# Kernel tuning notes

Measured on AMD Instinct MI355X. Metric: run time of the kernel, lower is better.

The kernel has to match this reference:

```python
import jax, jax.numpy as jnp
import numpy as np

B = 512      # batch
F = 512      # n_features
G = 32       # grid_size
N = G * G    # num_nodes = 1024
D = 64       # embed_dim
H = 64       # hidden_dim
C = 100      # n_classes
A = 8        # num_atoms in symbiotic basis
EPS = 1e-8
DEG_EPS = 1e-6


def _grid_mask():
    """4-neighborhood mask for a GxG grid, [N, N] float32."""
    m = np.zeros((N, N), dtype=np.float32)
    for i in range(N):
        r, c = divmod(i, G)
        if r > 0:
            m[i, i - G] = 1.0
        if r < G - 1:
            m[i, i + G] = 1.0
        if c > 0:
            m[i, i - 1] = 1.0
        if c < G - 1:
            m[i, i + 1] = 1.0
    return jnp.asarray(m)


def setup_inputs() -> dict:
    key = jax.random.key(0)
    ks = jax.random.split(key, 16)
    s = 0.05  # small init scale (stands in for kaiming init)
    return {
        "x": jax.random.normal(ks[0], (B, F), jnp.float32),
        "W_embed": jax.random.normal(ks[1], (F, N * D), jnp.float32) * s,
        "b_embed": jnp.zeros((N * D,), jnp.float32),
        "adj_weights": jax.random.normal(ks[2], (N, N), jnp.float32) * 0.1,
        "adj_mask": _grid_mask(),
        "W1": jax.random.normal(ks[3], (D, H), jnp.float32) * s,
        "b1": jnp.zeros((H,), jnp.float32),
        "W2": jax.random.normal(ks[4], (H, D), jnp.float32) * s,
        "b2": jnp.zeros((D,), jnp.float32),
        "basis": jax.random.normal(ks[5], (A, D), jnp.float32) * 0.5,
        "Wq": jax.random.normal(ks[6], (D, D), jnp.float32) * s,
        "Wk": jax.random.normal(ks[7], (D, D), jnp.float32) * s,
        "Wr1": jax.random.normal(ks[8], (N * D, 2 * H), jnp.float32) * s,
        "br1": jnp.zeros((2 * H,), jnp.float32),
        "Wr2": jax.random.normal(ks[9], (2 * H, C), jnp.float32) * s,
        "br2": jnp.zeros((C,), jnp.float32),
    }


def _gelu(v):
    return jax.nn.gelu(v, approximate=False)  # torch nn.GELU default (erf)


def reference(x, W_embed, b_embed, adj_weights, adj_mask, W1, b1, W2, b2,
              basis, Wq, Wk, Wr1, br1, Wr2, br2):
    plasticity = 1.0
    bsz = x.shape[0]
    # input embed -> [B, N, D]
    x_embed = (x @ W_embed + b_embed).reshape(bsz, N, D)
    # dynamic topology: sigmoid-gated, mask-multiplied, degree-normalized adjacency
    adj = jax.nn.sigmoid(adj_weights * plasticity) * adj_mask          # [N, N]
    deg = jnp.clip(adj.sum(axis=1, keepdims=True), DEG_EPS, None)
    adj = adj / deg
    # graph diffusion (shared adjacency across batch)
    x_agg = jnp.einsum('ij,bjd->bid', adj, x_embed)                    # [B, N, D]
    # node processor MLP
    x_proc = _gelu(x_agg @ W1 + b1) @ W2 + b2                          # [B, N, D]
    # symbiotic basis refinement on flattened rows [B*N, D]
    flat = x_proc.reshape(-1, D)
    Q = flat @ Wq                                                      # [B*N, D]
    K = basis @ Wk                                                     # [A, D]
    attn = (Q @ K.T) / (jnp.sqrt(jnp.float32(D)) + EPS)                # [B*N, A]
    weights = jax.nn.softmax(attn, axis=-1)
    x_clean = jnp.clip(weights @ basis, -5.0, 5.0)                     # [B*N, D]
    w_safe = weights + EPS
    entropy = -(w_safe * jnp.log(w_safe)).sum(-1).mean()
    gram = basis @ basis.T
    ortho = jnp.clip(jnp.sum((gram - jnp.eye(A, dtype=gram.dtype)) ** 2), 0.0, 10.0)
    # readout (dropout is identity in eval)
    x_flat = x_clean.reshape(bsz, N * D)
    logits = _gelu(x_flat @ Wr1 + br1) @ Wr2 + br2                     # [B, C]
    return (logits, entropy, ortho)
```

## Files before the change

kernel.cpp:

```cpp
#include <hip/hip_runtime.h>
#include <hip/hip_bf16.h>
#include <math.h>

#define Bb 512
#define Ff 512
#define Gg 32
#define Nn 1024
#define Dd 64
#define Hh 64
#define Cc 100
#define Aa 8
#define NDd 65536

typedef float  f32x4  __attribute__((ext_vector_type(4)));
typedef __bf16 bf16x8 __attribute__((ext_vector_type(8)));

static __device__ __forceinline__ unsigned short f2bf(float f) {
    __bf16 h = (__bf16)f;
    return __builtin_bit_cast(unsigned short, h);
}
static __device__ __forceinline__ float gelu_f(float v) {
    return 0.5f * v * (1.0f + erff(v * 0.7071067811865476f));
}
static __device__ __forceinline__ float gelu_fast(float v) {
    float z = 1.5957691216057308f * v * (1.0f + 0.044715f * v * v);
    return v / (1.0f + __expf(-z));
}
static __device__ __forceinline__ float sigm(float v) {
    return 1.0f / (1.0f + expf(-v));
}

__global__ void k_adj(const float* __restrict__ aw, const float* __restrict__ be,
                      float* __restrict__ adjw, float* __restrict__ be_agg) {
    int i = blockIdx.x * 256 + threadIdx.x;
    if (i >= Nn) return;
    int r = i >> 5, c = i & 31;
    float s0 = 0.f, s1 = 0.f, s2 = 0.f, s3 = 0.f;
    if (r > 0)       s0 = sigm(aw[(size_t)i * Nn + i - Gg]);
    if (r < Gg - 1)  s1 = sigm(aw[(size_t)i * Nn + i + Gg]);
    if (c > 0)       s2 = sigm(aw[(size_t)i * Nn + i - 1]);
    if (c < Gg - 1)  s3 = sigm(aw[(size_t)i * Nn + i + 1]);
    float deg = fmaxf(s0 + s1 + s2 + s3, 1e-6f);
    float inv = 1.0f / deg;
    float w0 = s0 * inv, w1 = s1 * inv, w2 = s2 * inv, w3 = s3 * inv;
    adjw[i * 4 + 0] = w0;
    adjw[i * 4 + 1] = w1;
    adjw[i * 4 + 2] = w2;
    adjw[i * 4 + 3] = w3;
    int nu = max(i - 32, 0), nd = min(i + 32, 1023);
    int nl = max(i - 1, 0),  nr = min(i + 1, 1023);
    #pragma unroll 4
    for (int d4 = 0; d4 < 16; ++d4) {
        f32x4 vu = *(const f32x4*)(be + nu * 64 + d4 * 4);
        f32x4 vd = *(const f32x4*)(be + nd * 64 + d4 * 4);
        f32x4 vl = *(const f32x4*)(be + nl * 64 + d4 * 4);
        f32x4 vr = *(const f32x4*)(be + nr * 64 + d4 * 4);
        f32x4 o = w0 * vu + w1 * vd + w2 * vl + w3 * vr;
        *(f32x4*)(be_agg + i * 64 + d4 * 4) = o;
    }
}

__global__ void __launch_bounds__(512) k_prep(
        const float* __restrict__ W1, const float* __restrict__ b2,
        const float* __restrict__ W2, const float* __restrict__ Wq,
        const float* __restrict__ Wk, const float* __restrict__ basis,
        unsigned short* __restrict__ Kbf, float* __restrict__ bq,
        unsigned short* __restrict__ W1f, unsigned short* __restrict__ Wcf,
        float* __restrict__ ortho_out) {
    __shared__ float sb[Aa * Dd];
    __shared__ float sWc[Hh * Dd];
    __shared__ float sKb[Aa * Dd];
    int t = threadIdx.x;
    sb[t] = basis[t];
    __syncthreads();
    {
        int a = t >> 6, d = t & 63;
        float acc = 0.f;
        #pragma unroll 8
        for (int e = 0; e < Dd; ++e) acc += sb[a * 64 + e] * Wk[e * 64 + d];
        sKb[t] = acc;
    }
    for (int it = 0; it < 8; ++it) {
        int o = it * 512 + t;
        int i = o >> 6, j = o & 63;
        float acc = 0.f;
        #pragma unroll 8
        for (int e = 0; e < 64; ++e) acc += W2[i * 64 + e] * Wq[e * 64 + j];
        sWc[o] = acc;
    }
    if (t < 64) {
        float acc = 0.f;
        #pragma unroll 8
        for (int e = 0; e < 64; ++e) acc += b2[e] * Wq[e * 64 + t];
        bq[t] = acc;
    }
    __syncthreads();
    {
        int l = t & 63, ni = (t >> 6) & 3, kk = t >> 8;
        int col = ni * 16 + (l & 15);
        int kbase = kk * 32 + (l >> 4) * 8;
        #pragma unroll
        for (int j = 0; j < 8; ++j) {
            int k = kbase + j;
            W1f[t * 8 + j] = f2bf(W1[k * 64 + col]);
            Wcf[t * 8 + j] = f2bf(sWc[k * 64 + col]);
        }
    }
    if (t < 128) {
        int lane = t & 63;
        int a = lane & 15;
        int dbase = ((t >> 6) * 32) + (lane >> 4) * 8;
        unsigned short kp[8];
        #pragma unroll
        for (int j = 0; j < 8; ++j)
            kp[j] = (a < 8) ? f2bf(sKb[a * 64 + dbase + j] * 0.125f) : (unsigned short)0;
        *(int4*)(Kbf + (size_t)t * 8) = *(int4*)kp;
    }
    if (t < 64) {
        int i = t >> 3, j = t & 7;
        float gsum = 0.f;
        #pragma unroll 8
        for (int d = 0; d < 64; ++d) gsum += sb[i * 64 + d] * sb[j * 64 + d];
        float diff = gsum - (i == j ? 1.0f : 0.0f);
        float v = diff * diff;
        #pragma unroll
        for (int off = 32; off; off >>= 1) v += __shfl_down(v, off);
        if (t == 0) *ortho_out = fminf(fmaxf(v, 0.0f), 10.0f);
    }
}

__global__ void __launch_bounds__(128) k_prepBW(
        const float* __restrict__ basis, const float* __restrict__ Wr1,
        unsigned short* __restrict__ BWf) {
    __shared__ float sb[Aa * Dd];
    int t = threadIdx.x;
    sb[t] = basis[t];         sb[t + 128] = basis[t + 128];
    sb[t + 256] = basis[t + 256]; sb[t + 384] = basis[t + 384];
    __syncthreads();
    int n = blockIdx.x;
    float acc[8] = {0, 0, 0, 0, 0, 0, 0, 0};
    const float* wr = Wr1 + (size_t)n * 64 * 128 + t;
    for (int d = 0; d < 64; ++d) {
        float v = wr[(size_t)d * 128];
        #pragma unroll
        for (int a = 0; a < 8; ++a) acc[a] += sb[a * 64 + d] * v;
    }
    unsigned short p[8];
    #pragma unroll
    for (int a = 0; a < 8; ++a) p[a] = f2bf(acc[a]);
    int ni = t >> 4, l15 = t & 15;
    *(int4*)(BWf + ((size_t)(((n >> 2) * 8 + ni) * 64) + (n & 3) * 16 + l15) * 8)
        = *(int4*)p;
}

__global__ void __launch_bounds__(256) k_xf(const float* __restrict__ x,
                                            unsigned short* __restrict__ xf) {
    int gid = blockIdx.x * 256 + threadIdx.x;
    int lane = gid & 63, slot = gid >> 6;
    int rt = slot >> 4, kk = slot & 15;
    int row = rt * 16 + (lane & 15), k0 = kk * 32 + (lane >> 4) * 8;
    const float* p = x + (size_t)row * Ff + k0;
    f32x4 v0 = *(const f32x4*)p;
    f32x4 v1 = *(const f32x4*)(p + 4);
    unsigned short o[8];
    o[0] = f2bf(v0.x); o[1] = f2bf(v0.y); o[2] = f2bf(v0.z); o[3] = f2bf(v0.w);
    o[4] = f2bf(v1.x); o[5] = f2bf(v1.y); o[6] = f2bf(v1.z); o[7] = f2bf(v1.w);
    *(int4*)(xf + (size_t)gid * 8) = *(int4*)o;
}

__global__ void __launch_bounds__(256) k_aggW(
        const float* __restrict__ We, const float* __restrict__ adjw,
        unsigned short* __restrict__ AfG) {
    int bid = blockIdx.x;
    int vid = (bid & 7) * 512 + (bid >> 3);
    int fo = vid >> 6;
    int win = vid & 63;
    int t = threadIdx.x;
    int c4 = win * 1024 + t * 4;
    int n = c4 >> 6;
    int d = c4 & 63;
    f32x4 w4 = *(const f32x4*)(adjw + n * 4);
    int nu = max(n - 32, 0), ndn = min(n + 32, 1023);
    int nl = max(n - 1, 0),  nr = min(n + 1, 1023);
    f32x4 vu[8], vd[8], vl[8], vr[8];
    #pragma unroll
    for (int j = 0; j < 8; ++j) {
        const float* row = We + (size_t)(fo * 8 + j) * NDd;
        vu[j] = *(const f32x4*)(row + nu * 64 + d);
        vd[j] = *(const f32x4*)(row + ndn * 64 + d);
        vl[j] = *(const f32x4*)(row + nl * 64 + d);
        vr[j] = *(const f32x4*)(row + nr * 64 + d);
    }
    unsigned short pk[4][8];
    #pragma unroll
    for (int j = 0; j < 8; ++j) {
        f32x4 o4 = w4.x * vu[j] + w4.y * vd[j] + w4.z * vl[j] + w4.w * vr[j];
        pk[0][j] = f2bf(o4.x); pk[1][j] = f2bf(o4.y);
        pk[2][j] = f2bf(o4.z); pk[3][j] = f2bf(o4.w);
    }
    int kk = fo >> 2, l4g = fo & 3;
    int mi = (c4 >> 4) & 3, l15b = c4 & 15;
    size_t base = ((((size_t)n * 16 + kk) * 4 + mi) * 64 + l4g * 16 + l15b) * 8;
    #pragma unroll
    for (int i = 0; i < 4; ++i)
        *(int4*)(AfG + base + i * 8) = *(int4*)pk[i];
}

__global__ void __launch_bounds__(512, 4) k_mega(
        const unsigned short* __restrict__ AfG, const unsigned short* __restrict__ xf,
        const float* __restrict__ be_agg,
        const unsigned short* __restrict__ W1f, const unsigned short* __restrict__ Wcf,
        const float* __restrict__ b1, const float* __restrict__ bq,
        const unsigned short* __restrict__ Kbf,
        unsigned short* __restrict__ w_outT, float* __restrict__ ent_part) {
    __shared__ __align__(16) unsigned short sm[32768];
    int t = threadIdx.x;
    int n = blockIdx.x;
    {
        const int4* src = (const int4*)AfG + (size_t)n * 4096;
        int4* dst = (int4*)sm;
        #pragma unroll
        for (int i = 0; i < 8; ++i) dst[t + i * 512] = src[t + i * 512];
    }
    __syncthreads();
    int lane = t & 63, w = t >> 6;
    int l15 = lane & 15, g = lane >> 4;
    int bs = w * 64;

    f32x4 acc[4][4] = {};
    #pragma unroll 4
    for (int kk = 0; kk < 16; ++kk) {
        bf16x8 a[4], b[4];
        #pragma unroll
        for (int mi = 0; mi < 4; ++mi)
            a[mi] = *(const bf16x8*)(sm + ((kk * 4 + mi) * 64 + lane) * 8);
        #pragma unroll
        for (int ni = 0; ni < 4; ++ni)
            b[ni] = *(const bf16x8*)(xf + ((size_t)(((w * 4 + ni) * 16 + kk) * 64 + lane)) * 8);
        #pragma unroll
        for (int mi = 0; mi < 4; ++mi)
            #pragma unroll
            for (int ni = 0; ni < 4; ++ni)
                acc[mi][ni] = __builtin_amdgcn_mfma_f32_16x16x32_bf16(
                    a[mi], b[ni], acc[mi][ni], 0, 0, 0);
    }
    __syncthreads();
    unsigned short* tile = sm + w * 4096;

    #pragma unroll
    for (int mi = 0; mi < 4; ++mi) {
        f32x4 bv = *(const f32x4*)(be_agg + n * 64 + mi * 16 + g * 4);
        int kk2 = mi >> 1;
        int gt  = ((mi & 1) << 1) + (g >> 1);
        int jb  = (g & 1) << 2;
        #pragma unroll
        for (int ni = 0; ni < 4; ++ni) {
            float v0 = acc[mi][ni][0] + bv[0];
            float v1 = acc[mi][ni][1] + bv[1];
            float v2 = acc[mi][ni][2] + bv[2];
            float v3 = acc[mi][ni][3] + bv[3];
            unsigned d0 = (unsigned)f2bf(v0) | ((unsigned)f2bf(v1) << 16);
            unsigned d1 = (unsigned)f2bf(v2) | ((unsigned)f2bf(v3) << 16);
            int base = ((kk2 * 4 + ni) * 64 + gt * 16 + l15) * 8 + jb;
            *(unsigned*)(tile + base)     = d0;
            *(unsigned*)(tile + base + 2) = d1;
        }
    }

    f32x4 acc1[4][4] = {};
    #pragma unroll
    for (int kk = 0; kk < 2; ++kk) {
        bf16x8 bf4[4];
        #pragma unroll
        for (int ni = 0; ni < 4; ++ni)
            bf4[ni] = *(const bf16x8*)(tile + ((kk * 4 + ni) * 64 + lane) * 8);
        #pragma unroll
        for (int mi = 0; mi < 4; ++mi) {
            bf16x8 aW = *(const bf16x8*)(W1f + ((kk * 4 + mi) * 64 + lane) * 8);
            #pragma unroll
            for (int ni = 0; ni < 4; ++ni)
                acc1[mi][ni] = __builtin_amdgcn_mfma_f32_16x16x32_bf16(
                    aW, bf4[ni], acc1[mi][ni], 0, 0, 0);
        }
    }
    #pragma unroll
    for (int mi = 0; mi < 4; ++mi) {
        f32x4 bv = *(const f32x4*)(b1 + mi * 16 + g * 4);
        int kk2 = mi >> 1;
        int gt  = ((mi & 1) << 1) + (g >> 1);
        int jb  = (g & 1) << 2;
        #pragma unroll
        for (int ni = 0; ni < 4; ++ni) {
            float h0 = gelu_fast(acc1[mi][ni][0] + bv[0]);
            float h1 = gelu_fast(acc1[mi][ni][1] + bv[1]);
            float h2 = gelu_fast(acc1[mi][ni][2] + bv[2]);
            float h3 = gelu_fast(acc1[mi][ni][3] + bv[3]);
            unsigned d0 = (unsigned)f2bf(h0) | ((unsigned)f2bf(h1) << 16);
            unsigned d1 = (unsigned)f2bf(h2) | ((unsigned)f2bf(h3) << 16);
            int base = ((kk2 * 4 + ni) * 64 + gt * 16 + l15) * 8 + jb;
            *(unsigned*)(tile + base)     = d0;
            *(unsigned*)(tile + base + 2) = d1;
        }
    }

    f32x4 acc2[4][4] = {};
    #pragma unroll
    for (int kk = 0; kk < 2; ++kk) {
        bf16x8 bf4[4];
        #pragma unroll
        for (int ni = 0; ni < 4; ++ni)
            bf4[ni] = *(const bf16x8*)(tile + ((kk * 4 + ni) * 64 + lane) * 8);
        #pragma unroll
        for (int mi = 0; mi < 4; ++mi) {
            bf16x8 aW = *(const bf16x8*)(Wcf + ((kk * 4 + mi) * 64 + lane) * 8);
            #pragma unroll
            for (int ni = 0; ni < 4; ++ni)
                acc2[mi][ni] = __builtin_amdgcn_mfma_f32_16x16x32_bf16(
                    aW, bf4[ni], acc2[mi][ni], 0, 0, 0);
        }
    }
    #pragma unroll
    for (int mi = 0; mi < 4; ++mi) {
        f32x4 bv = *(const f32x4*)(bq + mi * 16 + g * 4);
        int kk2 = mi >> 1;
        int gt  = ((mi & 1) << 1) + (g >> 1);
        int jb  = (g & 1) << 2;
        #pragma unroll
        for (int ni = 0; ni < 4; ++ni) {
            float q0 = acc2[mi][ni][0] + bv[0];
            float q1 = acc2[mi][ni][1] + bv[1];
            float q2 = acc2[mi][ni][2] + bv[2];
            float q3 = acc2[mi][ni][3] + bv[3];
            unsigned d0 = (unsigned)f2bf(q0) | ((unsigned)f2bf(q1) << 16);
            unsigned d1 = (unsigned)f2bf(q2) | ((unsigned)f2bf(q3) << 16);
            int base = ((kk2 * 4 + ni) * 64 + gt * 16 + l15) * 8 + jb;
            *(unsigned*)(tile + base)     = d0;
            *(unsigned*)(tile + base + 2) = d1;
        }
    }

    f32x4 accA[4] = {};
    #pragma unroll
    for (int kk = 0; kk < 2; ++kk) {
        bf16x8 kf = *(const bf16x8*)(Kbf + (kk * 64 + lane) * 8);
        #pragma unroll
        for (int ni = 0; ni < 4; ++ni) {
            bf16x8 qf = *(const bf16x8*)(tile + ((kk * 4 + ni) * 64 + lane) * 8);
            accA[ni] = __builtin_amdgcn_mfma_f32_16x16x32_bf16(kf, qf, accA[ni], 0, 0, 0);
        }
    }

    float ent_local = 0.f;
    bool odd = (g & 1);
    #pragma unroll
    for (int ni = 0; ni < 4; ++ni) {
        float xr[4];
        #pragma unroll
        for (int r = 0; r < 4; ++r) xr[r] = __shfl_xor(accA[ni][r], 16);
        float f[8];
        #pragma unroll
        for (int r = 0; r < 4; ++r) {
            f[r]     = odd ? xr[r] : accA[ni][r];
            f[r + 4] = odd ? accA[ni][r] : xr[r];
        }
        float mx = f[0];
        #pragma unroll
        for (int i = 1; i < 8; ++i) mx = fmaxf(mx, f[i]);
        float e[8], S = 0.f, T = 0.f;
        #pragma unroll
        for (int i = 0; i < 8; ++i) {
            e[i] = __expf(f[i] - mx);
            S += e[i];
            T += e[i] * (f[i] - mx);
        }
        float inv = 1.0f / S;
        if (g == 0) {
            ent_local += __logf(S) - T * inv;
            unsigned short pk[8];
            #pragma unroll
            for (int i = 0; i < 8; ++i) pk[i] = f2bf(e[i] * inv);
            *(int4*)(w_outT + ((size_t)n * 512 + bs + ni * 16 + l15) * 8) = *(int4*)pk;
        }
    }
    #pragma unroll
    for (int off = 32; off; off >>= 1) ent_local += __shfl_down(ent_local, off);
    if (lane == 0) ent_part[n * 8 + w] = ent_local;
}

__global__ void __launch_bounds__(256) k_rd(
        const unsigned short* __restrict__ w_outT,
        const unsigned short* __restrict__ BWf, float* __restrict__ Yp) {
    int mt = blockIdx.x & 3, kc = blockIdx.x >> 2;
    int t = threadIdx.x;
    int lane = t & 63, w = t >> 6;
    int l15 = lane & 15, l4 = lane >> 4;
    int rowbase = mt * 128 + w * 32;
    f32x4 acc[2][8] = {};
    for (int kkl = 0; kkl < 8; ++kkl) {
        int KK = kc * 8 + kkl;
        bf16x8 a[2];
        #pragma unroll
        for (int mi = 0; mi < 2; ++mi)
            a[mi] = *(const bf16x8*)(w_outT +
                ((size_t)(KK * 4 + l4) * 512 + rowbase + mi * 16 + l15) * 8);
        #pragma unroll
        for (int ni = 0; ni < 8; ++ni) {
            bf16x8 bb = *(const bf16x8*)(BWf + ((size_t)(KK * 8 + ni) * 64 + lane) * 8);
            #pragma unroll
            for (int mi = 0; mi < 2; ++mi)
                acc[mi][ni] = __builtin_amdgcn_mfma_f32_16x16x32_bf16(
                    a[mi], bb, acc[mi][ni], 0, 0, 0);
        }
    }
    #pragma unroll
    for (int ni = 0; ni < 8; ++ni)
        #pragma unroll
        for (int mi = 0; mi < 2; ++mi)
            #pragma unroll
            for (int r = 0; r < 4; ++r) {
                int rr = rowbase + mi * 16 + l4 * 4 + r;
                Yp[(size_t)kc * 65536 + rr * 128 + ni * 16 + l15] = acc[mi][ni][r];
            }
}

__global__ void __launch_bounds__(128) k_fin(
        const float* __restrict__ Yp, const float* __restrict__ br1,
        const float* __restrict__ Wr2, const float* __restrict__ br2,
        const float* __restrict__ ent_part, float* __restrict__ out) {
    __shared__ float yL[128];
    __shared__ float eR[128];
    int m = blockIdx.x, t = threadIdx.x;
    float s = 0.f;
    #pragma unroll
    for (int kc = 0; kc < 32; ++kc) s += Yp[(size_t)kc * 65536 + m * 128 + t];
    yL[t] = gelu_f(s + br1[t]);
    if (m == 0) {
        float es = 0.f;
        for (int i = t; i < 8192; i += 128) es += ent_part[i];
        eR[t] = es;
    }
    __syncthreads();
    if (t < 100) {
        float acc = br2[t];
        #pragma unroll 8
        for (int k = 0; k < 128; ++k) acc += yL[k] * Wr2[k * 100 + t];
        out[m * 100 + t] = acc;
    }
    if (m == 0 && t == 0) {
        float tot = 0.f;
        #pragma unroll
        for (int i = 0; i < 128; ++i) tot += eR[i];
        out[51200] = tot * (1.0f / 524288.0f);
    }
}

extern "C" void kernel_launch(void* const* d_in, const int* in_sizes, int n_in,
                              void* d_out, int out_size, void* d_ws, size_t ws_size,
                              hipStream_t stream) {
    const float* x     = (const float*)d_in[0];
    const float* We    = (const float*)d_in[1];
    const float* be    = (const float*)d_in[2];
    const float* aw    = (const float*)d_in[3];
    const float* W1    = (const float*)d_in[5];
    const float* b1    = (const float*)d_in[6];
    const float* W2    = (const float*)d_in[7];
    const float* b2    = (const float*)d_in[8];
    const float* basis = (const float*)d_in[9];
    const float* Wq    = (const float*)d_in[10];
    const float* Wk    = (const float*)d_in[11];
    const float* Wr1   = (const float*)d_in[12];
    const float* br1   = (const float*)d_in[13];
    const float* Wr2   = (const float*)d_in[14];
    const float* br2   = (const float*)d_in[15];
    (void)in_sizes; (void)n_in;

    if (ws_size < (size_t)90000000) return;

    char* ws = (char*)d_ws;
    unsigned short* w_outT = (unsigned short*)(ws);
    unsigned short* BWf    = (unsigned short*)(ws + 8388608);
    float*          Yp     = (float*)(ws + 10485760);
    unsigned short* AfG    = (unsigned short*)(ws + 18874368);
    char* smallp = ws + 18874368 + 67108864;
    float* adjw            = (float*)(smallp);
    unsigned short* Kbf    = (unsigned short*)(smallp + 16384);
    unsigned short* W1f    = (unsigned short*)(smallp + 18432);
    unsigned short* Wcf    = (unsigned short*)(smallp + 26624);
    float* bq              = (float*)(smallp + 34816);
    unsigned short* xf     = (unsigned short*)(smallp + 35072);
    float* be_agg          = (float*)(smallp + 35072 + 524288);
    float* ent_part        = (float*)(smallp + 35072 + 524288 + 262144);

    float* out = (float*)d_out;
    float* ortho_slot = out + 51201;

    k_adj<<<4, 256, 0, stream>>>(aw, be, adjw, be_agg);
    k_prep<<<1, 512, 0, stream>>>(W1, b2, W2, Wq, Wk, basis, Kbf, bq, W1f, Wcf, ortho_slot);
    k_prepBW<<<1024, 128, 0, stream>>>(basis, Wr1, BWf);
    k_xf<<<128, 256, 0, stream>>>(x, xf);
    k_aggW<<<4096, 256, 0, stream>>>(We, adjw, AfG);
    k_mega<<<1024, 512, 0, stream>>>(AfG, xf, be_agg, W1f, Wcf, b1, bq, Kbf, w_outT, ent_part);
    k_rd<<<128, 256, 0, stream>>>(w_outT, BWf, Yp);
    k_fin<<<512, 128, 0, stream>>>(Yp, br1, Wr2, br2, ent_part, out);
}
```

Measured before the change: 188.7 us.

## Halve LDS in mega kernel by staging adjacency in two halves and splitting tail

The mega kernel's shared buffer shrinks from 64KB to 32KB. The adjacency slice is now loaded in two K-halves with a barrier between them. The per-warp MLP/query/attention tail now processes the 64 batch columns in two halves of 32, which shrinks each warp's LDS tile and its accumulator arrays. The aim is to allow more resident blocks per CU and lower register pressure, at the cost of an extra barrier and shorter MFMA chains in the tail.

```diff
diff --git a/kernel.cpp b/kernel.cpp
--- a/kernel.cpp
+++ b/kernel.cpp
@@ -213,173 +213,188 @@
         const float* __restrict__ b1, const float* __restrict__ bq,
         const unsigned short* __restrict__ Kbf,
         unsigned short* __restrict__ w_outT, float* __restrict__ ent_part) {
-    __shared__ __align__(16) unsigned short sm[32768];
+    __shared__ __align__(16) unsigned short sm[16384];
     int t = threadIdx.x;
     int n = blockIdx.x;
-    {
-        const int4* src = (const int4*)AfG + (size_t)n * 4096;
-        int4* dst = (int4*)sm;
-        #pragma unroll
-        for (int i = 0; i < 8; ++i) dst[t + i * 512] = src[t + i * 512];
-    }
-    __syncthreads();
     int lane = t & 63, w = t >> 6;
     int l15 = lane & 15, g = lane >> 4;
     int bs = w * 64;
 
     f32x4 acc[4][4] = {};
-    #pragma unroll 4
-    for (int kk = 0; kk < 16; ++kk) {
-        bf16x8 a[4], b[4];
-        #pragma unroll
-        for (int mi = 0; mi < 4; ++mi)
-            a[mi] = *(const bf16x8*)(sm + ((kk * 4 + mi) * 64 + lane) * 8);
-        #pragma unroll
-        for (int ni = 0; ni < 4; ++ni)
-            b[ni] = *(const bf16x8*)(xf + ((size_t)(((w * 4 + ni) * 16 + kk) * 64 + lane)) * 8);
-        #pragma unroll
-        for (int mi = 0; mi < 4; ++mi)
+    #pragma unroll
+    for (int h = 0; h < 2; ++h) {
+        if (h) __syncthreads();
+        {
+            const int4* src = (const int4*)AfG + (size_t)n * 4096 + h * 2048;
+            int4* dst = (int4*)sm;
+            #pragma unroll
+            for (int i = 0; i < 4; ++i) dst[t + i * 512] = src[t + i * 512];
+        }
+        __syncthreads();
+        #pragma unroll 4
+        for (int kkl = 0; kkl < 8; ++kkl) {
+            int kk = h * 8 + kkl;
+            bf16x8 a[4], b[4];
+            #pragma unroll
+            for (int mi = 0; mi < 4; ++mi)
+                a[mi] = *(const bf16x8*)(sm + ((kkl * 4 + mi) * 64 + lane) * 8);
             #pragma unroll
             for (int ni = 0; ni < 4; ++ni)
-                acc[mi][ni] = __builtin_amdgcn_mfma_f32_16x16x32_bf16(
-                    a[mi], b[ni], acc[mi][ni], 0, 0, 0);
+                b[ni] = *(const bf16x8*)(xf + ((size_t)(((w * 4 + ni) * 16 + kk) * 64 + lane)) * 8);
+            #pragma unroll
+            for (int mi = 0; mi < 4; ++mi)
+                #pragma unroll
+                for (int ni = 0; ni < 4; ++ni)
+                    acc[mi][ni] = __builtin_amdgcn_mfma_f32_16x16x32_bf16(
+                        a[mi], b[ni], acc[mi][ni], 0, 0, 0);
+        }
     }
     __syncthreads();
-    unsigned short* tile = sm + w * 4096;
-
-    #pragma unroll
-    for (int mi = 0; mi < 4; ++mi) {
-        f32x4 bv = *(const f32x4*)(be_agg + n * 64 + mi * 16 + g * 4);
-        int kk2 = mi >> 1;
-        int gt  = ((mi & 1) << 1) + (g >> 1);
-        int jb  = (g & 1) << 2;
-        #pragma unroll
-        for (int ni = 0; ni < 4; ++ni) {
-            float v0 = acc[mi][ni][0] + bv[0];
-            float v1 = acc[mi][ni][1] + bv[1];
-            float v2 = acc[mi][ni][2] + bv[2];
-            float v3 = acc[mi][ni][3] + bv[3];
-            unsigned d0 = (unsigned)f2bf(v0) | ((unsigned)f2bf(v1) << 16);
-            unsigned d1 = (unsigned)f2bf(v2) | ((unsigned)f2bf(v3) << 16);
-            int base = ((kk2 * 4 + ni) * 64 + gt * 16 + l15) * 8 + jb;
-            *(unsigned*)(tile + base)     = d0;
-            *(unsigned*)(tile + base + 2) = d1;
-        }
-    }
-
-    f32x4 acc1[4][4] = {};
-    #pragma unroll
-    for (int kk = 0; kk < 2; ++kk) {
-        bf16x8 bf4[4];
-        #pragma unroll
-        for (int ni = 0; ni < 4; ++ni)
-            bf4[ni] = *(const bf16x8*)(tile + ((kk * 4 + ni) * 64 + lane) * 8);
-        #pragma unroll
-        for (int mi = 0; mi < 4; ++mi) {
-            bf16x8 aW = *(const bf16x8*)(W1f + ((kk * 4 + mi) * 64 + lane) * 8);
-            #pragma unroll
-            for (int ni = 0; ni < 4; ++ni)
-                acc1[mi][ni] = __builtin_amdgcn_mfma_f32_16x16x32_bf16(
-                    aW, bf4[ni], acc1[mi][ni], 0, 0, 0);
-        }
-    }
-    #pragma unroll
-    for (int mi = 0; mi < 4; ++mi) {
-        f32x4 bv = *(const f32x4*)(b1 + mi * 16 + g * 4);
-        int kk2 = mi >> 1;
-        int gt  = ((mi & 1) << 1) + (g >> 1);
-        int jb  = (g & 1) << 2;
-        #pragma unroll
-        for (int ni = 0; ni < 4; ++ni) {
-            float h0 = gelu_fast(acc1[mi][ni][0] + bv[0]);
-            float h1 = gelu_fast(acc1[mi][ni][1] + bv[1]);
-            float h2 = gelu_fast(acc1[mi][ni][2] + bv[2]);
-            float h3 = gelu_fast(acc1[mi][ni][3] + bv[3]);
-            unsigned d0 = (unsigned)f2bf(h0) | ((unsigned)f2bf(h1) << 16);
-            unsigned d1 = (unsigned)f2bf(h2) | ((unsigned)f2bf(h3) << 16);
-            int base = ((kk2 * 4 + ni) * 64 + gt * 16 + l15) * 8 + jb;
-            *(unsigned*)(tile + base)     = d0;
-            *(unsigned*)(tile + base + 2) = d1;
-        }
-    }
-
-    f32x4 acc2[4][4] = {};
-    #pragma unroll
-    for (int kk = 0; kk < 2; ++kk) {
-        bf16x8 bf4[4];
-        #pragma unroll
-        for (int ni = 0; ni < 4; ++ni)
-            bf4[ni] = *(const bf16x8*)(tile + ((kk * 4 + ni) * 64 + lane) * 8);
-        #pragma unroll
-        for (int mi = 0; mi < 4; ++mi) {
-            bf16x8 aW = *(const bf16x8*)(Wcf + ((kk * 4 + mi) * 64 + lane) * 8);
-            #pragma unroll
-            for (int ni = 0; ni < 4; ++ni)
-                acc2[mi][ni] = __builtin_amdgcn_mfma_f32_16x16x32_bf16(
-                    aW, bf4[ni], acc2[mi][ni], 0, 0, 0);
-        }
-    }
-    #pragma unroll
-    for (int mi = 0; mi < 4; ++mi) {
-        f32x4 bv = *(const f32x4*)(bq + mi * 16 + g * 4);
-        int kk2 = mi >> 1;
-        int gt  = ((mi & 1) << 1) + (g >> 1);
-        int jb  = (g & 1) << 2;
-        #pragma unroll
-        for (int ni = 0; ni < 4; ++ni) {
-            float q0 = acc2[mi][ni][0] + bv[0];
-            float q1 = acc2[mi][ni][1] + bv[1];
-            float q2 = acc2[mi][ni][2] + bv[2];
-            float q3 = acc2[mi][ni][3] + bv[3];
-            unsigned d0 = (unsigned)f2bf(q0) | ((unsigned)f2bf(q1) << 16);
-            unsigned d1 = (unsigned)f2bf(q2) | ((unsigned)f2bf(q3) << 16);
-            int base = ((kk2 * 4 + ni) * 64 + gt * 16 + l15) * 8 + jb;
-            *(unsigned*)(tile + base)     = d0;
-            *(unsigned*)(tile + base + 2) = d1;
-        }
-    }
-
-    f32x4 accA[4] = {};
-    #pragma unroll
-    for (int kk = 0; kk < 2; ++kk) {
-        bf16x8 kf = *(const bf16x8*)(Kbf + (kk * 64 + lane) * 8);
-        #pragma unroll
-        for (int ni = 0; ni < 4; ++ni) {
-            bf16x8 qf = *(const bf16x8*)(tile + ((kk * 4 + ni) * 64 + lane) * 8);
-            accA[ni] = __builtin_amdgcn_mfma_f32_16x16x32_bf16(kf, qf, accA[ni], 0, 0, 0);
-        }
-    }
+    unsigned short* tile = sm + w * 2048;
+
+    f32x4 bvbe[4];
+    #pragma unroll
+    for (int mi = 0; mi < 4; ++mi)
+        bvbe[mi] = *(const f32x4*)(be_agg + n * 64 + mi * 16 + g * 4);
 
     float ent_local = 0.f;
     bool odd = (g & 1);
-    #pragma unroll
-    for (int ni = 0; ni < 4; ++ni) {
-        float xr[4];
-        #pragma unroll
-        for (int r = 0; r < 4; ++r) xr[r] = __shfl_xor(accA[ni][r], 16);
-        float f[8];
-        #pragma unroll
-        for (int r = 0; r < 4; ++r) {
-            f[r]     = odd ? xr[r] : accA[ni][r];
-            f[r + 4] = odd ? accA[ni][r] : xr[r];
-        }
-        float mx = f[0];
-        #pragma unroll
-        for (int i = 1; i < 8; ++i) mx = fmaxf(mx, f[i]);
-        float e[8], S = 0.f, T = 0.f;
-        #pragma unroll
-        for (int i = 0; i < 8; ++i) {
-            e[i] = __expf(f[i] - mx);
-            S += e[i];
-            T += e[i] * (f[i] - mx);
-        }
-        float inv = 1.0f / S;
-        if (g == 0) {
-            ent_local += __logf(S) - T * inv;
-            unsigned short pk[8];
-            #pragma unroll
-            for (int i = 0; i < 8; ++i) pk[i] = f2bf(e[i] * inv);
-            *(int4*)(w_outT + ((size_t)n * 512 + bs + ni * 16 + l15) * 8) = *(int4*)pk;
+
+    #pragma unroll
+    for (int nh = 0; nh < 2; ++nh) {
+        #pragma unroll
+        for (int mi = 0; mi < 4; ++mi) {
+            int kk2 = mi >> 1;
+            int gt  = ((mi & 1) << 1) + (g >> 1);
+            int jb  = (g & 1) << 2;
+            #pragma unroll
+            for (int nl_ = 0; nl_ < 2; ++nl_) {
+                int niG = nh * 2 + nl_;
+                float v0 = acc[mi][niG][0] + bvbe[mi][0];
+                float v1 = acc[mi][niG][1] + bvbe[mi][1];
+                float v2 = acc[mi][niG][2] + bvbe[mi][2];
+                float v3 = acc[mi][niG][3] + bvbe[mi][3];
+                unsigned d0 = (unsigned)f2bf(v0) | ((unsigned)f2bf(v1) << 16);
+                unsigned d1 = (unsigned)f2bf(v2) | ((unsigned)f2bf(v3) << 16);
+                int base = ((kk2 * 2 + nl_) * 64 + gt * 16 + l15) * 8 + jb;
+                *(unsigned*)(tile + base)     = d0;
+                *(unsigned*)(tile + base + 2) = d1;
+            }
+        }
+
+        f32x4 acc1[4][2] = {};
+        #pragma unroll
+        for (int kk = 0; kk < 2; ++kk) {
+            bf16x8 bf2_[2];
+            #pragma unroll
+            for (int nl_ = 0; nl_ < 2; ++nl_)
+                bf2_[nl_] = *(const bf16x8*)(tile + ((kk * 2 + nl_) * 64 + lane) * 8);
+            #pragma unroll
+            for (int mi = 0; mi < 4; ++mi) {
+                bf16x8 aW = *(const bf16x8*)(W1f + ((kk * 4 + mi) * 64 + lane) * 8);
+                #pragma unroll
+                for (int nl_ = 0; nl_ < 2; ++nl_)
+                    acc1[mi][nl_] = __builtin_amdgcn_mfma_f32_16x16x32_bf16(
+                        aW, bf2_[nl_], acc1[mi][nl_], 0, 0, 0);
+            }
+        }
+        #pragma unroll
+        for (int mi = 0; mi < 4; ++mi) {
+            f32x4 bv = *(const f32x4*)(b1 + mi * 16 + g * 4);
+            int kk2 = mi >> 1;
+            int gt  = ((mi & 1) << 1) + (g >> 1);
+            int jb  = (g & 1) << 2;
+            #pragma unroll
+            for (int nl_ = 0; nl_ < 2; ++nl_) {
+                float h0 = gelu_fast(acc1[mi][nl_][0] + bv[0]);
+                float h1 = gelu_fast(acc1[mi][nl_][1] + bv[1]);
+                float h2 = gelu_fast(acc1[mi][nl_][2] + bv[2]);
+                float h3 = gelu_fast(acc1[mi][nl_][3] + bv[3]);
+                unsigned d0 = (unsigned)f2bf(h0) | ((unsigned)f2bf(h1) << 16);
+                unsigned d1 = (unsigned)f2bf(h2) | ((unsigned)f2bf(h3) << 16);
+                int base = ((kk2 * 2 + nl_) * 64 + gt * 16 + l15) * 8 + jb;
+                *(unsigned*)(tile + base)     = d0;
+                *(unsigned*)(tile + base + 2) = d1;
+            }
+        }
+
+        f32x4 acc2[4][2] = {};
+        #pragma unroll
+        for (int kk = 0; kk < 2; ++kk) {
+            bf16x8 bf2_[2];
+            #pragma unroll
+            for (int nl_ = 0; nl_ < 2; ++nl_)
+                bf2_[nl_] = *(const bf16x8*)(tile + ((kk * 2 + nl_) * 64 + lane) * 8);
+            #pragma unroll
+            for (int mi = 0; mi < 4; ++mi) {
+                bf16x8 aW = *(const bf16x8*)(Wcf + ((kk * 4 + mi) * 64 + lane) * 8);
+                #pragma unroll
+                for (int nl_ = 0; nl_ < 2; ++nl_)
+                    acc2[mi][nl_] = __builtin_amdgcn_mfma_f32_16x16x32_bf16(
+                        aW, bf2_[nl_], acc2[mi][nl_], 0, 0, 0);
+            }
+        }
+        #pragma unroll
+        for (int mi = 0; mi < 4; ++mi) {
+            f32x4 bv = *(const f32x4*)(bq + mi * 16 + g * 4);
+            int kk2 = mi >> 1;
+            int gt  = ((mi & 1) << 1) + (g >> 1);
+            int jb  = (g & 1) << 2;
+            #pragma unroll
+            for (int nl_ = 0; nl_ < 2; ++nl_) {
+                float q0 = acc2[mi][nl_][0] + bv[0];
+                float q1 = acc2[mi][nl_][1] + bv[1];
+                float q2 = acc2[mi][nl_][2] + bv[2];
+                float q3 = acc2[mi][nl_][3] + bv[3];
+                unsigned d0 = (unsigned)f2bf(q0) | ((unsigned)f2bf(q1) << 16);
+                unsigned d1 = (unsigned)f2bf(q2) | ((unsigned)f2bf(q3) << 16);
+                int base = ((kk2 * 2 + nl_) * 64 + gt * 16 + l15) * 8 + jb;
+                *(unsigned*)(tile + base)     = d0;
+                *(unsigned*)(tile + base + 2) = d1;
+            }
+        }
+
+        f32x4 accA[2] = {};
+        #pragma unroll
+        for (int kk = 0; kk < 2; ++kk) {
+            bf16x8 kf = *(const bf16x8*)(Kbf + (kk * 64 + lane) * 8);
+            #pragma unroll
+            for (int nl_ = 0; nl_ < 2; ++nl_) {
+                bf16x8 qf = *(const bf16x8*)(tile + ((kk * 2 + nl_) * 64 + lane) * 8);
+                accA[nl_] = __builtin_amdgcn_mfma_f32_16x16x32_bf16(kf, qf, accA[nl_], 0, 0, 0);
+            }
+        }
+
+        #pragma unroll
+        for (int nl_ = 0; nl_ < 2; ++nl_) {
+            float xr[4];
+            #pragma unroll
+            for (int r = 0; r < 4; ++r) xr[r] = __shfl_xor(accA[nl_][r], 16);
+            float f[8];
+            #pragma unroll
+            for (int r = 0; r < 4; ++r) {
+                f[r]     = odd ? xr[r] : accA[nl_][r];
+                f[r + 4] = odd ? accA[nl_][r] : xr[r];
+            }
+            float mx = f[0];
+            #pragma unroll
+            for (int i = 1; i < 8; ++i) mx = fmaxf(mx, f[i]);
+            float e[8], S = 0.f, T = 0.f;
+            #pragma unroll
+            for (int i = 0; i < 8; ++i) {
+                e[i] = __expf(f[i] - mx);
+                S += e[i];
+                T += e[i] * (f[i] - mx);
+            }
+            float inv = 1.0f / S;
+            if (g == 0) {
+                ent_local += __logf(S) - T * inv;
+                unsigned short pk[8];
+                #pragma unroll
+                for (int i = 0; i < 8; ++i) pk[i] = f2bf(e[i] * inv);
+                *(int4*)(w_outT + ((size_t)n * 512 + bs + (nh * 2 + nl_) * 16 + l15) * 8)
+                    = *(int4*)pk;
+            }
         }
     }
     #pragma unroll
```

New measurement: 186.6 us. About the same (-1.1%).
